# Kernel tuning notes

Hardware: AMD Instinct MI355X
Metric: run time of the kernel (lower is better)

## Reference

```python
import jax, jax.numpy as jnp
import numpy as np

D_MODEL = 1024
NUM_HEAD = 16
HEAD_DIM = D_MODEL // NUM_HEAD  # 64


def setup_inputs() -> dict:
    key = jax.random.key(0)
    ks = jax.random.split(key, 9)
    B, S = 2, 2048
    s = 0.02
    return {
        "x": jax.random.normal(ks[0], (B, S, D_MODEL), dtype=jnp.float32),
        "Wq": jax.random.normal(ks[1], (D_MODEL, D_MODEL), dtype=jnp.float32) * s,
        "bq": jax.random.normal(ks[2], (D_MODEL,), dtype=jnp.float32) * s,
        "Wk": jax.random.normal(ks[3], (D_MODEL, D_MODEL), dtype=jnp.float32) * s,
        "bk": jax.random.normal(ks[4], (D_MODEL,), dtype=jnp.float32) * s,
        "Wv": jax.random.normal(ks[5], (D_MODEL, D_MODEL), dtype=jnp.float32) * s,
        "bv": jax.random.normal(ks[6], (D_MODEL,), dtype=jnp.float32) * s,
        "Wo": jax.random.normal(ks[7], (D_MODEL, D_MODEL), dtype=jnp.float32) * s,
        "bo": jax.random.normal(ks[8], (D_MODEL,), dtype=jnp.float32) * s,
    }


def _split_head(t):
    # [B,S,D] -> [B,H,S,hd]
    B, S, _ = t.shape
    return t.reshape(B, S, NUM_HEAD, HEAD_DIM).transpose(0, 2, 1, 3)


def reference(x, Wq, bq, Wk, bk, Wv, bv, Wo, bo):
    B, S, D = x.shape
    q = _split_head(x @ Wq.T + bq)  # [B,H,S,hd]
    k = _split_head(x @ Wk.T + bk)
    v = _split_head(x @ Wv.T + bv)
    scale = 1.0 / jnp.sqrt(jnp.asarray(HEAD_DIM, dtype=x.dtype))
    scores = jnp.einsum("bhqd,bhkd->bhqk", q, k) * scale  # [B,H,S,S]
    attn = jax.nn.softmax(scores, axis=-1)
    out = jnp.einsum("bhqk,bhkd->bhqd", attn, v)  # [B,H,S,hd]
    out = out.transpose(0, 2, 1, 3).reshape(B, S, D)
    return out @ Wo.T + bo
```

## Files before the change

### kernel.cpp

```cpp
#include <hip/hip_runtime.h>
#include <cstdint>


typedef unsigned short ush;
typedef __bf16 bf16x8 __attribute__((ext_vector_type(8)));
typedef float f32x4 __attribute__((ext_vector_type(4)));
typedef ush u16x8 __attribute__((ext_vector_type(8)));
typedef ush u16x4 __attribute__((ext_vector_type(4)));
typedef unsigned int u32x4 __attribute__((ext_vector_type(4)));

__device__ __forceinline__ ush f2bf(float f) {
  unsigned int u = __float_as_uint(f);
  u += 0x7fffu + ((u >> 16) & 1u);
  return (ush)(u >> 16);
}

__device__ __forceinline__ unsigned int pack2bf_ru(float a, float b) {
  unsigned int ua = __float_as_uint(a) + 0x8000u;
  unsigned int ub = __float_as_uint(b) + 0x8000u;
  return __builtin_amdgcn_perm(ub, ua, 0x07060302u);
}

__device__ __forceinline__ bf16x8 bc8(u16x8 v) {
  return __builtin_bit_cast(bf16x8, v);
}

__device__ __forceinline__ void async16(const void* g, void* l) {
  __builtin_amdgcn_global_load_lds(
      (const __attribute__((address_space(1))) unsigned int*)(uintptr_t)g,
      (__attribute__((address_space(3))) unsigned int*)(uintptr_t)l, 16, 0, 0);
}

__global__ __launch_bounds__(256) void convert_kernel(
    const float* __restrict__ x, const float* __restrict__ Wq,
    const float* __restrict__ Wk, const float* __restrict__ Wv,
    const float* __restrict__ Wo,
    ush* __restrict__ xb, ush* __restrict__ Wqb, ush* __restrict__ Wkb,
    ush* __restrict__ Wvb, ush* __restrict__ Wob)
{
  int tid = blockIdx.x * 256 + threadIdx.x;
  int base = tid * 4;
  const float* src; ush* dst; int idx;
  if (base < 4194304) { src = x; dst = xb; idx = base; }
  else {
    int r = base - 4194304;
    int seg = r >> 20;
    idx = r & 1048575;
    src = seg == 0 ? Wq : seg == 1 ? Wk : seg == 2 ? Wv : Wo;
    dst = seg == 0 ? Wqb : seg == 1 ? Wkb : seg == 2 ? Wvb : Wob;
  }
  float4 f = *(const float4*)(src + idx);
  u16x4 u = { f2bf(f.x), f2bf(f.y), f2bf(f.z), f2bf(f.w) };
  *(u16x4*)(dst + idx) = u;
}

__device__ __forceinline__ void gemm128_core(
    const ush* __restrict__ gA, const ush* __restrict__ gB,
    int m0, int n0, ush* lA, ush* lB, f32x4 (&acc)[4][4])
{
  const int t = threadIdx.x, w = t >> 6, lane = t & 63;
  const int l15 = lane & 15, quad = lane >> 4;
  const int wm = (w >> 1) * 64, wn = (w & 1) * 64;
#pragma unroll
  for (int i = 0; i < 4; ++i)
#pragma unroll
    for (int j = 0; j < 4; ++j) acc[i][j] = (f32x4){0.f, 0.f, 0.f, 0.f};

  for (int kt = 0; kt < 1024; kt += 64) {
#pragma unroll
    for (int i = 0; i < 4; ++i) {
      int j = i * 256 + w * 64 + lane;
      int row = j >> 3, cc = (j & 7) ^ (row & 7);
      async16(gA + (size_t)(m0 + row) * 1024 + kt + cc * 8,
              lA + (i * 256 + w * 64) * 8);
    }
#pragma unroll
    for (int i = 0; i < 4; ++i) {
      int j = i * 256 + w * 64 + lane;
      int row = j >> 3, cc = (j & 7) ^ (row & 7);
      async16(gB + (size_t)(n0 + row) * 1024 + kt + cc * 8,
              lB + (i * 256 + w * 64) * 8);
    }
    __syncthreads();
#pragma unroll
    for (int kf = 0; kf < 2; ++kf) {
      bf16x8 aF[4], bF[4];
#pragma unroll
      for (int mt = 0; mt < 4; ++mt) {
        int row = wm + mt * 16 + l15;
        aF[mt] = bc8(*(const u16x8*)(lA + row * 64 + (((kf * 4 + quad) ^ (row & 7)) * 8)));
      }
#pragma unroll
      for (int nt = 0; nt < 4; ++nt) {
        int row = wn + nt * 16 + l15;
        bF[nt] = bc8(*(const u16x8*)(lB + row * 64 + (((kf * 4 + quad) ^ (row & 7)) * 8)));
      }
#pragma unroll
      for (int mt = 0; mt < 4; ++mt)
#pragma unroll
        for (int nt = 0; nt < 4; ++nt)
          acc[mt][nt] = __builtin_amdgcn_mfma_f32_16x16x32_bf16(
              aF[mt], bF[nt], acc[mt][nt], 0, 0, 0);
    }
    __syncthreads();
  }
}

__global__ __launch_bounds__(256, 2) void qkv_gemm(
    const ush* __restrict__ xb, const ush* __restrict__ Wqb,
    const ush* __restrict__ Wkb, const ush* __restrict__ Wvb,
    const float* __restrict__ bq, const float* __restrict__ bk,
    const float* __restrict__ bv,
    ush* __restrict__ q, ush* __restrict__ k, ush* __restrict__ vt)
{
  int bid = blockIdx.x;
  int wsel = bid >> 8;
  int rem = bid & 255;
  int m0 = (rem & 31) * 128;
  int n0 = (rem >> 5) * 128;
  const ush* gB = wsel == 0 ? Wqb : wsel == 1 ? Wkb : Wvb;
  const float* bias = wsel == 0 ? bq : wsel == 1 ? bk : bv;
  const float oscale = wsel == 1 ? 0.180336880f : 1.0f;

  __shared__ alignas(16) ush lA[128 * 64];
  __shared__ alignas(16) ush lB[128 * 64];
  f32x4 acc[4][4];
  gemm128_core(xb, gB, m0, n0, lA, lB, acc);

  const int t = threadIdx.x, w = t >> 6, lane = t & 63;
  const int l15 = lane & 15, quad = lane >> 4;
  const int wm = (w >> 1) * 64, wn = (w & 1) * 64;
  if (wsel == 2) {
#pragma unroll
    for (int nt = 0; nt < 4; ++nt) {
      int o = n0 + wn + nt * 16 + l15;
      float bl = bias[o];
      int h = o >> 6, d = o & 63;
#pragma unroll
      for (int mt = 0; mt < 4; ++mt) {
        int tb = m0 + wm + mt * 16 + quad * 4;
        int b = tb >> 11, s = tb & 2047;
        int so = s & 63;
        int sp = (s & ~63) | (so & 35) | ((so & 12) << 1) | ((so & 16) >> 2);
        u16x4 pk = { f2bf(acc[mt][nt][0] + bl), f2bf(acc[mt][nt][1] + bl),
                     f2bf(acc[mt][nt][2] + bl), f2bf(acc[mt][nt][3] + bl) };
        *(u16x4*)(vt + (size_t)(((b * 16 + h) * 64) + d) * 2048 + sp) = pk;
      }
    }
  } else {
    ush* dst = wsel == 0 ? q : k;
#pragma unroll
    for (int nt = 0; nt < 4; ++nt) {
      int o = n0 + wn + nt * 16 + l15;
      float bl = bias[o];
      int h = o >> 6, d = o & 63;
#pragma unroll
      for (int mt = 0; mt < 4; ++mt)
#pragma unroll
        for (int r = 0; r < 4; ++r) {
          int token = m0 + wm + mt * 16 + quad * 4 + r;
          int b = token >> 11, s = token & 2047;
          dst[(size_t)(((b * 16 + h) * 2048) + s) * 64 + d] =
              f2bf((acc[mt][nt][r] + bl) * oscale);
        }
    }
  }
}

__global__ __launch_bounds__(256, 4) void attn_kernel(
    const ush* __restrict__ Q, const ush* __restrict__ K,
    const ush* __restrict__ VT, ush* __restrict__ O)
{
  const int bid = blockIdx.x;
  const int bh = (bid & 7) * 4 + (bid >> 8);
  const int qt = (bid >> 3) & 31;
  const ush* qb = Q + (size_t)bh * 2048 * 64;
  const ush* kb = K + (size_t)bh * 2048 * 64;
  const ush* vtb = VT + (size_t)bh * 64 * 2048;
  const int t = threadIdx.x, w = t >> 6, lane = t & 63;
  const int wk = w & 1, wq = w >> 1;
  const int l15 = lane & 15, quad = lane >> 4;
  const int q0 = qt * 64 + wq * 32;

  __shared__ alignas(16) ush lK[2][64 * 64];
  __shared__ alignas(16) ush lV[2][64 * 64];

  const int r0 = t >> 3;
  const int c0 = (t & 7) ^ (r0 & 7);
  const ush* kSrc = kb + (size_t)r0 * 64 + c0 * 8;
  const ush* vSrc = vtb + (size_t)r0 * 2048 + c0 * 8;

  bf16x8 qF[2][2];
#pragma unroll
  for (int g = 0; g < 2; ++g)
#pragma unroll
    for (int kf = 0; kf < 2; ++kf)
      qF[g][kf] = bc8(*(const u16x8*)(qb + (size_t)(q0 + g * 16 + l15) * 64 +
                                      kf * 32 + quad * 8));

  float li[2] = {0.f, 0.f};
  f32x4 accO[2][4];
#pragma unroll
  for (int g = 0; g < 2; ++g)
#pragma unroll
    for (int dt = 0; dt < 4; ++dt) accO[g][dt] = (f32x4){0.f, 0.f, 0.f, 0.f};

#pragma unroll
  for (int i = 0; i < 2; ++i) {
    async16(kSrc + i * 2048, lK[0] + (i * 256 + t) * 8);
    async16(vSrc + (size_t)i * 32 * 2048, lV[0] + (i * 256 + t) * 8);
  }
  __syncthreads();

  for (int it = 0; it < 32; ++it) {
    const int cur = it & 1, nxt = cur ^ 1;
    if (it + 1 < 32) {
      const size_t ko = (size_t)(it + 1) * 64 * 64;
      const int vo = (it + 1) * 64;
#pragma unroll
      for (int i = 0; i < 2; ++i) {
        async16(kSrc + ko + i * 2048, lK[nxt] + (i * 256 + t) * 8);
        async16(vSrc + vo + (size_t)i * 32 * 2048, lV[nxt] + (i * 256 + t) * 8);
      }
    }
    const ush* lk = lK[cur];
    const ush* lv = lV[cur];

    f32x4 sc[2][2];
#pragma unroll
    for (int g = 0; g < 2; ++g)
#pragma unroll
      for (int mt = 0; mt < 2; ++mt) sc[g][mt] = (f32x4){0.f, 0.f, 0.f, 0.f};
#pragma unroll
    for (int kf = 0; kf < 2; ++kf) {
#pragma unroll
      for (int mt = 0; mt < 2; ++mt) {
        int row = (2 * wk + mt) * 16 + l15;
        bf16x8 aK = bc8(*(const u16x8*)(lk + row * 64 + (((kf * 4 + quad) ^ (row & 7)) * 8)));
#pragma unroll
        for (int g = 0; g < 2; ++g)
          sc[g][mt] = __builtin_amdgcn_mfma_f32_16x16x32_bf16(
              aK, qF[g][kf], sc[g][mt], 0, 0, 0);
      }
    }

#pragma unroll
    for (int g = 0; g < 2; ++g) {
      float rs = 0.f;
#pragma unroll
      for (int mt = 0; mt < 2; ++mt)
#pragma unroll
        for (int r = 0; r < 4; ++r) {
          sc[g][mt][r] = __builtin_amdgcn_exp2f(sc[g][mt][r]);
          rs += sc[g][mt][r];
        }
      li[g] += rs;
    }

    bf16x8 aV[4];
#pragma unroll
    for (int dt = 0; dt < 4; ++dt)
      aV[dt] = bc8(*(const u16x8*)(lv + (dt * 16 + l15) * 64 +
                                   (((wk * 4 + quad) ^ (l15 & 7)) * 8)));
#pragma unroll
    for (int g = 0; g < 2; ++g) {
      u32x4 bw = { pack2bf_ru(sc[g][0][0], sc[g][0][1]),
                   pack2bf_ru(sc[g][0][2], sc[g][0][3]),
                   pack2bf_ru(sc[g][1][0], sc[g][1][1]),
                   pack2bf_ru(sc[g][1][2], sc[g][1][3]) };
      bf16x8 bP = __builtin_bit_cast(bf16x8, bw);
#pragma unroll
      for (int dt = 0; dt < 4; ++dt)
        accO[g][dt] = __builtin_amdgcn_mfma_f32_16x16x32_bf16(
            aV[dt], bP, accO[g][dt], 0, 0, 0);
    }
    __syncthreads();
  }

#pragma unroll
  for (int g = 0; g < 2; ++g) {
    li[g] += __shfl_xor(li[g], 16);
    li[g] += __shfl_xor(li[g], 32);
  }

  float* redO = (float*)lK;
  float* redL = (float*)lV;
  const int b = bh >> 4, h = bh & 15;
#define SEND_GROUP(GL)                                                       \
  {                                                                          \
    const int Gs = 2 * wq + (GL);                                            \
    _Pragma("unroll")                                                        \
    for (int dt = 0; dt < 4; ++dt)                                           \
      *(f32x4*)(redO + ((Gs * 4 + dt) * 64 + lane) * 4) = accO[GL][dt];      \
    redL[Gs * 64 + lane] = li[GL];                                           \
  }
#define FINISH_GROUP(GL)                                                     \
  {                                                                          \
    const int Gf = 2 * wq + (GL);                                            \
    _Pragma("unroll")                                                        \
    for (int dt = 0; dt < 4; ++dt)                                           \
      accO[GL][dt] += *(const f32x4*)(redO + ((Gf * 4 + dt) * 64 + lane) * 4);\
    float lsum = li[GL] + redL[Gf * 64 + lane];                              \
    const float linv = __builtin_amdgcn_rcpf(lsum);                          \
    const int s = q0 + (GL) * 16 + l15;                                      \
    _Pragma("unroll")                                                        \
    for (int dt = 0; dt < 4; ++dt) {                                         \
      u16x4 pk = { f2bf(accO[GL][dt][0] * linv), f2bf(accO[GL][dt][1] * linv),\
                   f2bf(accO[GL][dt][2] * linv), f2bf(accO[GL][dt][3] * linv)};\
      *(u16x4*)(O + (size_t)(b * 2048 + s) * 1024 + h * 64 + dt * 16 +       \
                quad * 4) = pk;                                              \
    }                                                                        \
  }
  if (wk == 0) { SEND_GROUP(1); } else { SEND_GROUP(0); }
  __syncthreads();
  if (wk == 0) { FINISH_GROUP(0); } else { FINISH_GROUP(1); }
#undef SEND_GROUP
#undef FINISH_GROUP
}

__global__ __launch_bounds__(256, 2) void out_gemm(
    const ush* __restrict__ ab, const ush* __restrict__ Wob,
    const float* __restrict__ bo, float* __restrict__ out)
{
  int rem = blockIdx.x;
  int m0 = (rem & 31) * 128;
  int n0 = (rem >> 5) * 128;
  __shared__ alignas(16) ush lA[128 * 64];
  __shared__ alignas(16) ush lB[128 * 64];
  f32x4 acc[4][4];
  gemm128_core(ab, Wob, m0, n0, lA, lB, acc);

  const int t = threadIdx.x, w = t >> 6, lane = t & 63;
  const int l15 = lane & 15, quad = lane >> 4;
  const int wm = (w >> 1) * 64, wn = (w & 1) * 64;
#pragma unroll
  for (int nt = 0; nt < 4; ++nt) {
    int o = n0 + wn + nt * 16 + l15;
    float bl = bo[o];
#pragma unroll
    for (int mt = 0; mt < 4; ++mt)
#pragma unroll
      for (int r = 0; r < 4; ++r) {
        int token = m0 + wm + mt * 16 + quad * 4 + r;
        out[(size_t)token * 1024 + o] = acc[mt][nt][r] + bl;
      }
  }
}

extern "C" void kernel_launch(void* const* d_in, const int* in_sizes, int n_in,
                              void* d_out, int out_size, void* d_ws, size_t ws_size,
                              hipStream_t stream)
{
  const float* x  = (const float*)d_in[0];
  const float* Wq = (const float*)d_in[1];
  const float* bq = (const float*)d_in[2];
  const float* Wk = (const float*)d_in[3];
  const float* bk = (const float*)d_in[4];
  const float* Wv = (const float*)d_in[5];
  const float* bv = (const float*)d_in[6];
  const float* Wo = (const float*)d_in[7];
  const float* bo = (const float*)d_in[8];
  float* out = (float*)d_out;

  char* ws = (char*)d_ws;
  ush* xb  = (ush*)(ws);
  ush* Wqb = (ush*)(ws + (size_t)( 8u << 20));
  ush* Wkb = (ush*)(ws + (size_t)(10u << 20));
  ush* Wvb = (ush*)(ws + (size_t)(12u << 20));
  ush* Wob = (ush*)(ws + (size_t)(14u << 20));
  ush* qb  = (ush*)(ws + (size_t)(16u << 20));
  ush* kb  = (ush*)(ws + (size_t)(24u << 20));
  ush* vtb = (ush*)(ws + (size_t)(32u << 20));
  ush* ab  = (ush*)(ws + (size_t)(40u << 20));

  convert_kernel<<<8192, 256, 0, stream>>>(x, Wq, Wk, Wv, Wo,
                                           xb, Wqb, Wkb, Wvb, Wob);
  qkv_gemm<<<768, 256, 0, stream>>>(xb, Wqb, Wkb, Wvb, bq, bk, bv, qb, kb, vtb);
  attn_kernel<<<1024, 256, 0, stream>>>(qb, kb, vtb, ab);
  out_gemm<<<256, 256, 0, stream>>>(ab, Wob, bo, out);
}
```

Before: 184.3 us.

## Compute softmax row sums via MFMA, use hardware bf16 pack, retile out GEMM

The attention kernel now accumulates the softmax denominator with an extra MFMA against a ones vector, replacing the per-element scalar adds and the final cross-lane shuffles. The manual round-up bf16 packing is replaced with the v_cvt_pk_bf16_f32 instruction. The output projection GEMM switches from 128x128 tiles to 128x64 tiles with its own unpipelined load loop, launching 512 blocks instead of 256 for better CU occupancy. The denominator now sums the bf16-rounded probabilities, which matches what feeds the PV product. The cost is one extra MFMA per group per iteration and a GEMM loop with no double buffering.

```diff
diff --git a/kernel.cpp b/kernel.cpp
--- a/kernel.cpp
+++ b/kernel.cpp
@@ -15,10 +15,10 @@
   return (ush)(u >> 16);
 }
 
-__device__ __forceinline__ unsigned int pack2bf_ru(float a, float b) {
-  unsigned int ua = __float_as_uint(a) + 0x8000u;
-  unsigned int ub = __float_as_uint(b) + 0x8000u;
-  return __builtin_amdgcn_perm(ub, ua, 0x07060302u);
+__device__ __forceinline__ unsigned int cvtpk2bf(float a, float b) {
+  unsigned int r;
+  asm("v_cvt_pk_bf16_f32 %0, %1, %2" : "=v"(r) : "v"(a), "v"(b));
+  return r;
 }
 
 __device__ __forceinline__ bf16x8 bc8(u16x8 v) {
@@ -198,12 +198,18 @@
       qF[g][kf] = bc8(*(const u16x8*)(qb + (size_t)(q0 + g * 16 + l15) * 64 +
                                       kf * 32 + quad * 8));
 
-  float li[2] = {0.f, 0.f};
+  const u16x8 onesU = { 0x3F80, 0x3F80, 0x3F80, 0x3F80,
+                        0x3F80, 0x3F80, 0x3F80, 0x3F80 };
+  const bf16x8 aOnes = bc8(onesU);
+
   f32x4 accO[2][4];
-#pragma unroll
-  for (int g = 0; g < 2; ++g)
+  f32x4 accLi[2];
+#pragma unroll
+  for (int g = 0; g < 2; ++g) {
+    accLi[g] = (f32x4){0.f, 0.f, 0.f, 0.f};
 #pragma unroll
     for (int dt = 0; dt < 4; ++dt) accO[g][dt] = (f32x4){0.f, 0.f, 0.f, 0.f};
+  }
 
 #pragma unroll
   for (int i = 0; i < 2; ++i) {
@@ -245,17 +251,12 @@
     }
 
 #pragma unroll
-    for (int g = 0; g < 2; ++g) {
-      float rs = 0.f;
+    for (int g = 0; g < 2; ++g)
 #pragma unroll
       for (int mt = 0; mt < 2; ++mt)
 #pragma unroll
-        for (int r = 0; r < 4; ++r) {
+        for (int r = 0; r < 4; ++r)
           sc[g][mt][r] = __builtin_amdgcn_exp2f(sc[g][mt][r]);
-          rs += sc[g][mt][r];
-        }
-      li[g] += rs;
-    }
 
     bf16x8 aV[4];
 #pragma unroll
@@ -264,23 +265,19 @@
                                    (((wk * 4 + quad) ^ (l15 & 7)) * 8)));
 #pragma unroll
     for (int g = 0; g < 2; ++g) {
-      u32x4 bw = { pack2bf_ru(sc[g][0][0], sc[g][0][1]),
-                   pack2bf_ru(sc[g][0][2], sc[g][0][3]),
-                   pack2bf_ru(sc[g][1][0], sc[g][1][1]),
-                   pack2bf_ru(sc[g][1][2], sc[g][1][3]) };
+      u32x4 bw = { cvtpk2bf(sc[g][0][0], sc[g][0][1]),
+                   cvtpk2bf(sc[g][0][2], sc[g][0][3]),
+                   cvtpk2bf(sc[g][1][0], sc[g][1][1]),
+                   cvtpk2bf(sc[g][1][2], sc[g][1][3]) };
       bf16x8 bP = __builtin_bit_cast(bf16x8, bw);
+      accLi[g] = __builtin_amdgcn_mfma_f32_16x16x32_bf16(
+          aOnes, bP, accLi[g], 0, 0, 0);
 #pragma unroll
       for (int dt = 0; dt < 4; ++dt)
         accO[g][dt] = __builtin_amdgcn_mfma_f32_16x16x32_bf16(
             aV[dt], bP, accO[g][dt], 0, 0, 0);
     }
     __syncthreads();
-  }
-
-#pragma unroll
-  for (int g = 0; g < 2; ++g) {
-    li[g] += __shfl_xor(li[g], 16);
-    li[g] += __shfl_xor(li[g], 32);
   }
 
   float* redO = (float*)lK;
@@ -292,7 +289,7 @@
     _Pragma("unroll")                                                        \
     for (int dt = 0; dt < 4; ++dt)                                           \
       *(f32x4*)(redO + ((Gs * 4 + dt) * 64 + lane) * 4) = accO[GL][dt];      \
-    redL[Gs * 64 + lane] = li[GL];                                           \
+    redL[Gs * 64 + lane] = accLi[GL][0];                                     \
   }
 #define FINISH_GROUP(GL)                                                     \
   {                                                                          \
@@ -300,7 +297,7 @@
     _Pragma("unroll")                                                        \
     for (int dt = 0; dt < 4; ++dt)                                           \
       accO[GL][dt] += *(const f32x4*)(redO + ((Gf * 4 + dt) * 64 + lane) * 4);\
-    float lsum = li[GL] + redL[Gf * 64 + lane];                              \
+    float lsum = accLi[GL][0] + redL[Gf * 64 + lane];                        \
     const float linv = __builtin_amdgcn_rcpf(lsum);                          \
     const int s = q0 + (GL) * 16 + l15;                                      \
     _Pragma("unroll")                                                        \
@@ -324,17 +321,61 @@
 {
   int rem = blockIdx.x;
   int m0 = (rem & 31) * 128;
-  int n0 = (rem >> 5) * 128;
+  int n0 = (rem >> 5) * 64;
   __shared__ alignas(16) ush lA[128 * 64];
-  __shared__ alignas(16) ush lB[128 * 64];
-  f32x4 acc[4][4];
-  gemm128_core(ab, Wob, m0, n0, lA, lB, acc);
+  __shared__ alignas(16) ush lB[64 * 64];
 
   const int t = threadIdx.x, w = t >> 6, lane = t & 63;
   const int l15 = lane & 15, quad = lane >> 4;
-  const int wm = (w >> 1) * 64, wn = (w & 1) * 64;
-#pragma unroll
-  for (int nt = 0; nt < 4; ++nt) {
+  const int wm = (w >> 1) * 64, wn = (w & 1) * 32;
+
+  f32x4 acc[4][2];
+#pragma unroll
+  for (int i = 0; i < 4; ++i)
+#pragma unroll
+    for (int j = 0; j < 2; ++j) acc[i][j] = (f32x4){0.f, 0.f, 0.f, 0.f};
+
+  for (int kt = 0; kt < 1024; kt += 64) {
+#pragma unroll
+    for (int i = 0; i < 4; ++i) {
+      int j = i * 256 + w * 64 + lane;
+      int row = j >> 3, cc = (j & 7) ^ (row & 7);
+      async16(ab + (size_t)(m0 + row) * 1024 + kt + cc * 8,
+              lA + (i * 256 + w * 64) * 8);
+    }
+#pragma unroll
+    for (int i = 0; i < 2; ++i) {
+      int j = i * 256 + w * 64 + lane;
+      int row = j >> 3, cc = (j & 7) ^ (row & 7);
+      async16(Wob + (size_t)(n0 + row) * 1024 + kt + cc * 8,
+              lB + (i * 256 + w * 64) * 8);
+    }
+    __syncthreads();
+#pragma unroll
+    for (int kf = 0; kf < 2; ++kf) {
+      bf16x8 aF[4], bF[2];
+#pragma unroll
+      for (int mt = 0; mt < 4; ++mt) {
+        int row = wm + mt * 16 + l15;
+        aF[mt] = bc8(*(const u16x8*)(lA + row * 64 + (((kf * 4 + quad) ^ (row & 7)) * 8)));
+      }
+#pragma unroll
+      for (int nt = 0; nt < 2; ++nt) {
+        int row = wn + nt * 16 + l15;
+        bF[nt] = bc8(*(const u16x8*)(lB + row * 64 + (((kf * 4 + quad) ^ (row & 7)) * 8)));
+      }
+#pragma unroll
+      for (int mt = 0; mt < 4; ++mt)
+#pragma unroll
+        for (int nt = 0; nt < 2; ++nt)
+          acc[mt][nt] = __builtin_amdgcn_mfma_f32_16x16x32_bf16(
+              aF[mt], bF[nt], acc[mt][nt], 0, 0, 0);
+    }
+    __syncthreads();
+  }
+
+#pragma unroll
+  for (int nt = 0; nt < 2; ++nt) {
     int o = n0 + wn + nt * 16 + l15;
     float bl = bo[o];
 #pragma unroll
@@ -377,5 +418,5 @@
                                            xb, Wqb, Wkb, Wvb, Wob);
   qkv_gemm<<<768, 256, 0, stream>>>(xb, Wqb, Wkb, Wvb, bq, bk, bv, qb, kb, vtb);
   attn_kernel<<<1024, 256, 0, stream>>>(qb, kb, vtb, ab);
-  out_gemm<<<256, 256, 0, stream>>>(ab, Wob, bo, out);
-}
+  out_gemm<<<512, 256, 0, stream>>>(ab, Wob, bo, out);
+}
```

Result: faster. 175.5 us (-4.8%).
